# Performance work log

Measured on AMD Instinct MI355X. Metric: run time of the kernel, lower is better.

The kernel has to match this reference:

```python
import jax, jax.numpy as jnp
import numpy as np

N_NODES = 50000
N_EDGES = 800000
IN_CH = 128
HID = 64
OUT_CH = 2
NEG_SLOPE = 0.2


def gcn_conv(x, src, dst, deg_isqrt, W, b):
    # PyG GCNConv: x @ W, symmetric normalization with self-loops, scatter-add, + bias
    h = x @ W  # [N, HID]
    norm = deg_isqrt[src] * deg_isqrt[dst]  # [E+N]
    msg = h[src] * norm[:, None]  # gather + scale
    out = jax.ops.segment_sum(msg, dst, num_segments=x.shape[0])
    return out + b


def setup_inputs() -> dict:
    key = jax.random.key(0)
    ks = jax.random.split(key, 16)
    glorot = lambda k, i, o: jax.random.normal(k, (i, o), jnp.float32) * jnp.sqrt(2.0 / (i + o))
    inp = {
        "node_features": jax.random.normal(ks[0], (N_NODES, IN_CH), jnp.float32),
        "edge_index": jax.random.randint(ks[1], (2, N_EDGES), 0, N_NODES, jnp.int64 if jax.config.jax_enable_x64 else jnp.int32),
        "fc1_W": glorot(ks[2], IN_CH, 32), "fc1_b": jnp.zeros((32,), jnp.float32),
        "fc2_W": glorot(ks[3], 32, HID), "fc2_b": jnp.zeros((HID,), jnp.float32),
        "conv1_W": glorot(ks[4], HID, HID), "conv1_b": jnp.zeros((HID,), jnp.float32),
        "conv2_W": glorot(ks[5], HID, HID), "conv2_b": jnp.zeros((HID,), jnp.float32),
        "conv3_W": glorot(ks[6], HID, HID), "conv3_b": jnp.zeros((HID,), jnp.float32),
        "conv4_W": glorot(ks[7], HID, HID), "conv4_b": jnp.zeros((HID,), jnp.float32),
        "final_W": glorot(ks[8], HID, OUT_CH), "final_b": jnp.zeros((OUT_CH,), jnp.float32),
    }
    return inp


def reference(node_features, edge_index, fc1_W, fc1_b, fc2_W, fc2_b,
              conv1_W, conv1_b, conv2_W, conv2_b, conv3_W, conv3_b,
              conv4_W, conv4_b, final_W, final_b):
    N = node_features.shape[0]
    # add self-loops once (shared by all conv layers)
    loops = jnp.arange(N, dtype=edge_index.dtype)
    src = jnp.concatenate([edge_index[0], loops])
    dst = jnp.concatenate([edge_index[1], loops])
    deg = jax.ops.segment_sum(jnp.ones_like(dst, jnp.float32), dst, num_segments=N)
    deg_isqrt = jnp.where(deg > 0, jax.lax.rsqrt(jnp.maximum(deg, 1.0)), 0.0)

    lrelu = lambda x: jnp.where(x >= 0, x, NEG_SLOPE * x)

    x = jax.nn.relu(node_features @ fc1_W + fc1_b) @ fc2_W + fc2_b  # fc stack
    out1 = lrelu(gcn_conv(x, src, dst, deg_isqrt, conv1_W, conv1_b))
    out2 = lrelu(gcn_conv(out1, src, dst, deg_isqrt, conv2_W, conv2_b)) + out1
    out3 = lrelu(gcn_conv(out2, src, dst, deg_isqrt, conv3_W, conv3_b))
    out4 = gcn_conv(out3, src, dst, deg_isqrt, conv4_W, conv4_b) + out2
    return out4 @ final_W + final_b
```

## Files before the change

kernel.cpp:

```cpp
#include <hip/hip_runtime.h>

#define NN 50000
#define NE 800000
#define HIST_BLOCKS ((NE + 255) / 256)
#define FILL_BLOCKS HIST_BLOCKS
#define FC_BLOCKS 1024

typedef unsigned short u16;
typedef unsigned int u32;

__device__ inline float rlf(float v, int l) {
    return __int_as_float(__builtin_amdgcn_readlane(__float_as_int(v), l));
}
__device__ inline u16 f2bf(float f) {
    u32 u = __float_as_uint(f);
    u32 r = (u + 0x7FFFu + ((u >> 16) & 1u)) >> 16;
    return (u16)r;
}
__device__ inline float lo16(u32 q) { return __uint_as_float(q << 16); }
__device__ inline float hi16(u32 q) { return __uint_as_float(q & 0xffff0000u); }

__global__ __launch_bounds__(256) void k_hist_foldw(
    const int* __restrict__ dst, int* __restrict__ cnt,
    const float* __restrict__ fc2W, const float* __restrict__ b2,
    const float* __restrict__ c1W, float* __restrict__ W2c,
    float* __restrict__ b2c) {
    if (blockIdx.x < HIST_BLOCKS) {
        int e = blockIdx.x * 256 + threadIdx.x;
        if (e < NE) atomicAdd(&cnt[dst[e]], 1);
    } else {
        int j = (blockIdx.x - HIST_BLOCKS) * 4 + (threadIdx.x >> 6);
        int c = threadIdx.x & 63;
        if (j < 32) {
            float s = 0.f;
            for (int k = 0; k < 64; ++k) s = fmaf(fc2W[j * 64 + k], c1W[k * 64 + c], s);
            W2c[j * 64 + c] = s;
        } else if (j == 32) {
            float s = 0.f;
            for (int k = 0; k < 64; ++k) s = fmaf(b2[k], c1W[k * 64 + c], s);
            b2c[c] = s;
        }
    }
}

__global__ __launch_bounds__(1024) void k_scan(int* __restrict__ cnt,
                                               int* __restrict__ rowptr,
                                               float* __restrict__ disq) {
    __shared__ int wsum[16];
    __shared__ int carry;
    int t = threadIdx.x, wave = t >> 6, lane = t & 63;
    if (t == 0) { carry = 0; rowptr[0] = 0; }
    __syncthreads();
    for (int base = 0; base < NN; base += 1024) {
        int i = base + t;
        int x = (i < NN) ? cnt[i] : 0;
        if (i < NN) {
            cnt[i] = 0;
            disq[i] = rsqrtf((float)x + 1.0f);
        }
        for (int off = 1; off < 64; off <<= 1) {
            int y = __shfl_up(x, off, 64);
            if (lane >= off) x += y;
        }
        if (lane == 63) wsum[wave] = x;
        __syncthreads();
        if (wave == 0 && lane < 16) {
            int w = wsum[lane];
            for (int off = 1; off < 16; off <<= 1) {
                int y = __shfl_up(w, off, 16);
                if (lane >= off) w += y;
            }
            wsum[lane] = w;
        }
        __syncthreads();
        int incl = carry + ((wave > 0) ? wsum[wave - 1] : 0) + x;
        if (i < NN) rowptr[i + 1] = incl;
        __syncthreads();
        if (t == 1023) carry = incl;
        __syncthreads();
    }
}

__global__ __launch_bounds__(256) void k_fill_fc(
    const int* __restrict__ src, const int* __restrict__ dst,
    const int* __restrict__ rowptr, int* __restrict__ cur,
    u16* __restrict__ esrc,
    const float* __restrict__ nf,
    const float* __restrict__ W1, const float* __restrict__ b1,
    const float* __restrict__ W2c, const float* __restrict__ b2c,
    const float* __restrict__ disq, u16* __restrict__ Hb) {
    if (blockIdx.x < FILL_BLOCKS) {
        int e = blockIdx.x * 256 + threadIdx.x;
        if (e < NE) {
            int d = dst[e];
            int pos = rowptr[d] + atomicAdd(&cur[d], 1);
            esrc[pos] = (u16)src[e];
        }
        return;
    }
    int lane = threadIdx.x & 63;
    int c = lane & 31, h = lane >> 5;
    int wid = ((blockIdx.x - FILL_BLOCKS) * 256 + threadIdx.x) >> 6;
    int nwaves = (FC_BLOCKS * 256) >> 6;
    float w1[64], w2[32];
    #pragma unroll
    for (int j = 0; j < 64; ++j) w1[j] = W1[(h * 64 + j) * 32 + c];
    #pragma unroll
    for (int j = 0; j < 32; ++j) w2[j] = W2c[j * 64 + lane];
    float b1c = b1[c], b2l = b2c[lane];
    for (int n = wid; n < NN; n += nwaves) {
        float x0 = nf[(size_t)n * 128 + lane];
        float x1 = nf[(size_t)n * 128 + 64 + lane];
        float s = 0.f;
        #pragma unroll
        for (int j = 0; j < 64; ++j) {
            float xa = rlf(x0, j), xb = rlf(x1, j);
            s = fmaf(h ? xb : xa, w1[j], s);
        }
        s += __shfl_xor(s, 32, 64);
        float hv = fmaxf(s + b1c, 0.f);
        float o = b2l;
        #pragma unroll
        for (int j = 0; j < 32; ++j) o = fmaf(rlf(hv, j), w2[j], o);
        Hb[(size_t)n * 64 + lane] = f2bf(disq[n] * o);
    }
}

__global__ __launch_bounds__(256) void k_gemm64(
    const float* __restrict__ X, const float* __restrict__ W,
    const float* __restrict__ disq, u16* __restrict__ Hb) {
    int lane = threadIdx.x & 63;
    int wid = (blockIdx.x * 256 + threadIdx.x) >> 6;
    int nwaves = (gridDim.x * 256) >> 6;
    float wcol[64];
    #pragma unroll
    for (int k = 0; k < 64; ++k) wcol[k] = W[k * 64 + lane];
    for (int n = wid; n < NN; n += nwaves) {
        float xv = X[(size_t)n * 64 + lane];
        float acc = 0.f;
        #pragma unroll
        for (int k = 0; k < 64; ++k) acc = fmaf(rlf(xv, k), wcol[k], acc);
        Hb[(size_t)n * 64 + lane] = f2bf(disq[n] * acc);
    }
}

__global__ __launch_bounds__(256) void k_csr_conv(
    const u16* __restrict__ Hb, const int* __restrict__ rowptr,
    const u16* __restrict__ esrc, const float* __restrict__ disq,
    const float* __restrict__ b, const float* __restrict__ res,
    float* __restrict__ out, int do_lrelu) {
    int lane = threadIdx.x & 63;
    int half = lane >> 5;
    int cl = (lane & 31) * 2;
    int n = (blockIdx.x * 256 + threadIdx.x) >> 6;
    if (n >= NN) return;
    int beg = rowptr[n], end = rowptr[n + 1];
    float a0 = 0.f, a1 = 0.f;
    for (int base = beg; base < end; base += 64) {
        int cnt = min(64, end - base);
        int idx = (lane < cnt) ? (int)esrc[base + lane] : 0;
        int j = 0;
        for (; j + 8 <= cnt; j += 8) {
            int p0 = __builtin_amdgcn_readlane(idx, j + 0);
            int p1 = __builtin_amdgcn_readlane(idx, j + 1);
            int p2 = __builtin_amdgcn_readlane(idx, j + 2);
            int p3 = __builtin_amdgcn_readlane(idx, j + 3);
            int p4 = __builtin_amdgcn_readlane(idx, j + 4);
            int p5 = __builtin_amdgcn_readlane(idx, j + 5);
            int p6 = __builtin_amdgcn_readlane(idx, j + 6);
            int p7 = __builtin_amdgcn_readlane(idx, j + 7);
            int sA = half ? p1 : p0;
            int sB = half ? p3 : p2;
            int sC = half ? p5 : p4;
            int sD = half ? p7 : p6;
            u32 qA = *(const u32*)(Hb + ((size_t)sA * 64 + cl));
            u32 qB = *(const u32*)(Hb + ((size_t)sB * 64 + cl));
            u32 qC = *(const u32*)(Hb + ((size_t)sC * 64 + cl));
            u32 qD = *(const u32*)(Hb + ((size_t)sD * 64 + cl));
            a0 += (lo16(qA) + lo16(qB)) + (lo16(qC) + lo16(qD));
            a1 += (hi16(qA) + hi16(qB)) + (hi16(qC) + hi16(qD));
        }
        for (; j + 2 <= cnt; j += 2) {
            int p0 = __builtin_amdgcn_readlane(idx, j);
            int p1 = __builtin_amdgcn_readlane(idx, j + 1);
            int s = half ? p1 : p0;
            u32 q = *(const u32*)(Hb + ((size_t)s * 64 + cl));
            a0 += lo16(q);
            a1 += hi16(q);
        }
        if (j < cnt) {
            int s = __builtin_amdgcn_readlane(idx, j);
            if (!half) {
                u32 q = *(const u32*)(Hb + ((size_t)s * 64 + cl));
                a0 += lo16(q);
                a1 += hi16(q);
            }
        }
    }
    a0 += __shfl_xor(a0, 32, 64);
    a1 += __shfl_xor(a1, 32, 64);
    u32 qs = *(const u32*)(Hb + ((size_t)n * 64 + cl));
    a0 += lo16(qs);
    a1 += hi16(qs);
    float dn = disq[n];
    float v0 = dn * a0 + b[cl];
    float v1 = dn * a1 + b[cl + 1];
    if (do_lrelu) {
        v0 = (v0 >= 0.f) ? v0 : 0.2f * v0;
        v1 = (v1 >= 0.f) ? v1 : 0.2f * v1;
    }
    if (res) {
        float2 r = *(const float2*)(res + ((size_t)n * 64 + cl));
        v0 += r.x;
        v1 += r.y;
    }
    if (!half) {
        float2 o;
        o.x = v0;
        o.y = v1;
        *(float2*)(out + ((size_t)n * 64 + cl)) = o;
    }
}

__global__ __launch_bounds__(256) void k_csr_conv_final(
    const u16* __restrict__ Hb, const int* __restrict__ rowptr,
    const u16* __restrict__ esrc, const float* __restrict__ disq,
    const float* __restrict__ b, const float* __restrict__ res,
    const float* __restrict__ FW, const float* __restrict__ fb,
    float* __restrict__ out) {
    int lane = threadIdx.x & 63;
    int half = lane >> 5;
    int cl = (lane & 31) * 2;
    int n = (blockIdx.x * 256 + threadIdx.x) >> 6;
    if (n >= NN) return;
    int beg = rowptr[n], end = rowptr[n + 1];
    float a0 = 0.f, a1 = 0.f;
    for (int base = beg; base < end; base += 64) {
        int cnt = min(64, end - base);
        int idx = (lane < cnt) ? (int)esrc[base + lane] : 0;
        int j = 0;
        for (; j + 8 <= cnt; j += 8) {
            int p0 = __builtin_amdgcn_readlane(idx, j + 0);
            int p1 = __builtin_amdgcn_readlane(idx, j + 1);
            int p2 = __builtin_amdgcn_readlane(idx, j + 2);
            int p3 = __builtin_amdgcn_readlane(idx, j + 3);
            int p4 = __builtin_amdgcn_readlane(idx, j + 4);
            int p5 = __builtin_amdgcn_readlane(idx, j + 5);
            int p6 = __builtin_amdgcn_readlane(idx, j + 6);
            int p7 = __builtin_amdgcn_readlane(idx, j + 7);
            int sA = half ? p1 : p0;
            int sB = half ? p3 : p2;
            int sC = half ? p5 : p4;
            int sD = half ? p7 : p6;
            u32 qA = *(const u32*)(Hb + ((size_t)sA * 64 + cl));
            u32 qB = *(const u32*)(Hb + ((size_t)sB * 64 + cl));
            u32 qC = *(const u32*)(Hb + ((size_t)sC * 64 + cl));
            u32 qD = *(const u32*)(Hb + ((size_t)sD * 64 + cl));
            a0 += (lo16(qA) + lo16(qB)) + (lo16(qC) + lo16(qD));
            a1 += (hi16(qA) + hi16(qB)) + (hi16(qC) + hi16(qD));
        }
        for (; j + 2 <= cnt; j += 2) {
            int p0 = __builtin_amdgcn_readlane(idx, j);
            int p1 = __builtin_amdgcn_readlane(idx, j + 1);
            int s = half ? p1 : p0;
            u32 q = *(const u32*)(Hb + ((size_t)s * 64 + cl));
            a0 += lo16(q);
            a1 += hi16(q);
        }
        if (j < cnt) {
            int s = __builtin_amdgcn_readlane(idx, j);
            if (!half) {
                u32 q = *(const u32*)(Hb + ((size_t)s * 64 + cl));
                a0 += lo16(q);
                a1 += hi16(q);
            }
        }
    }
    a0 += __shfl_xor(a0, 32, 64);
    a1 += __shfl_xor(a1, 32, 64);
    u32 qs = *(const u32*)(Hb + ((size_t)n * 64 + cl));
    a0 += lo16(qs);
    a1 += hi16(qs);
    float dn = disq[n];
    float2 r = *(const float2*)(res + ((size_t)n * 64 + cl));
    float v0 = dn * a0 + b[cl] + r.x;
    float v1 = dn * a1 + b[cl + 1] + r.y;
    float p0 = v0 * FW[cl * 2 + 0] + v1 * FW[(cl + 1) * 2 + 0];
    float p1 = v0 * FW[cl * 2 + 1] + v1 * FW[(cl + 1) * 2 + 1];
    for (int off = 16; off; off >>= 1) {
        p0 += __shfl_xor(p0, off, 64);
        p1 += __shfl_xor(p1, off, 64);
    }
    if (lane == 0) {
        out[n * 2 + 0] = p0 + fb[0];
        out[n * 2 + 1] = p1 + fb[1];
    }
}

extern "C" void kernel_launch(void* const* d_in, const int* in_sizes, int n_in,
                              void* d_out, int out_size, void* d_ws, size_t ws_size,
                              hipStream_t stream) {
    const float* nf   = (const float*)d_in[0];
    const int*   ei   = (const int*)d_in[1];
    const float* fc1W = (const float*)d_in[2];
    const float* fc1b = (const float*)d_in[3];
    const float* fc2W = (const float*)d_in[4];
    const float* fc2b = (const float*)d_in[5];
    const float* cW[4] = {(const float*)d_in[6], (const float*)d_in[8],
                          (const float*)d_in[10], (const float*)d_in[12]};
    const float* cb[4] = {(const float*)d_in[7], (const float*)d_in[9],
                          (const float*)d_in[11], (const float*)d_in[13]};
    const float* fW = (const float*)d_in[14];
    const float* fb = (const float*)d_in[15];
    const int* src = ei;
    const int* dst = ei + NE;

    float* ws     = (float*)d_ws;
    float* disq   = ws;
    int*   cnt    = (int*)(ws + 50048);
    int*   rowptr = cnt + 50048;
    u16*   esrc   = (u16*)(rowptr + 50056);
    float* W2c    = (float*)(esrc + 800000);
    float* b2c    = W2c + 2048;
    float* B0     = b2c + 64;
    float* B1     = B0 + (size_t)NN * 64;
    u16*   Hb     = (u16*)(B1 + (size_t)NN * 64);

    hipMemsetAsync(cnt, 0, 50048 * sizeof(int), stream);
    k_hist_foldw<<<HIST_BLOCKS + 9, 256, 0, stream>>>(dst, cnt, fc2W, fc2b, cW[0],
                                                      W2c, b2c);
    k_scan<<<1, 1024, 0, stream>>>(cnt, rowptr, disq);
    k_fill_fc<<<FILL_BLOCKS + FC_BLOCKS, 256, 0, stream>>>(
        src, dst, rowptr, cnt, esrc, nf, fc1W, fc1b, W2c, b2c, disq, Hb);

    const int cgrid = (NN * 64 + 255) / 256;

    k_csr_conv<<<cgrid, 256, 0, stream>>>(Hb, rowptr, esrc, disq, cb[0], nullptr, B1, 1);
    k_gemm64<<<512, 256, 0, stream>>>(B1, cW[1], disq, Hb);
    k_csr_conv<<<cgrid, 256, 0, stream>>>(Hb, rowptr, esrc, disq, cb[1], B1, B0, 1);
    k_gemm64<<<512, 256, 0, stream>>>(B0, cW[2], disq, Hb);
    k_csr_conv<<<cgrid, 256, 0, stream>>>(Hb, rowptr, esrc, disq, cb[2], nullptr, B1, 1);
    k_gemm64<<<512, 256, 0, stream>>>(B1, cW[3], disq, Hb);
    k_csr_conv_final<<<cgrid, 256, 0, stream>>>(Hb, rowptr, esrc, disq, cb[3], B0,
                                                fW, fb, (float*)d_out);
}
```

Measured before the change: 353.4 us.

## Gather 4 edges per wave step with 8-byte loads and zero padding row

The CSR aggregation kernels now split each wave into four 16-lane quarters. Each quarter gathers a different neighbour row with an 8-byte load of 4 bf16 channels, instead of two halves each doing 4-byte loads. Out-of-range edge slots point at a zeroed padding row at index NN, which removes the tail branches, and the cross-quarter reduction uses two shuffles. The fill/fc kernel also interleaves its FC blocks among the fill blocks so the two kinds of work run together. This adds extra shuffles and padding-row loads on partial groups, and relies on the workspace having room for the extra Hb row.

After: 428.7 us. 1.21x slower.

```diff
diff --git a/kernel.cpp b/kernel.cpp
--- a/kernel.cpp
+++ b/kernel.cpp
@@ -45,11 +45,13 @@
 
 __global__ __launch_bounds__(1024) void k_scan(int* __restrict__ cnt,
                                                int* __restrict__ rowptr,
-                                               float* __restrict__ disq) {
+                                               float* __restrict__ disq,
+                                               u16* __restrict__ Hb) {
     __shared__ int wsum[16];
     __shared__ int carry;
     int t = threadIdx.x, wave = t >> 6, lane = t & 63;
     if (t == 0) { carry = 0; rowptr[0] = 0; }
+    if (t < 64) Hb[(size_t)NN * 64 + t] = 0;
     __syncthreads();
     for (int base = 0; base < NN; base += 1024) {
         int i = base + t;
@@ -89,8 +91,11 @@
     const float* __restrict__ W1, const float* __restrict__ b1,
     const float* __restrict__ W2c, const float* __restrict__ b2c,
     const float* __restrict__ disq, u16* __restrict__ Hb) {
-    if (blockIdx.x < FILL_BLOCKS) {
-        int e = blockIdx.x * 256 + threadIdx.x;
+    int b = blockIdx.x;
+    bool is_fc = ((b & 3) == 3) && ((b >> 2) < FC_BLOCKS);
+    if (!is_fc) {
+        int fillIdx = b - min(b >> 2, FC_BLOCKS);
+        int e = fillIdx * 256 + threadIdx.x;
         if (e < NE) {
             int d = dst[e];
             int pos = rowptr[d] + atomicAdd(&cur[d], 1);
@@ -100,7 +105,7 @@
     }
     int lane = threadIdx.x & 63;
     int c = lane & 31, h = lane >> 5;
-    int wid = ((blockIdx.x - FILL_BLOCKS) * 256 + threadIdx.x) >> 6;
+    int wid = ((b >> 2) * 256 + threadIdx.x) >> 6;
     int nwaves = (FC_BLOCKS * 256) >> 6;
     float w1[64], w2[32];
     #pragma unroll
@@ -144,81 +149,65 @@
     }
 }
 
+#define GRP(J)                                                              \
+    {                                                                       \
+        int p0 = __builtin_amdgcn_readlane(idx, (J) + 0);                   \
+        int p1 = __builtin_amdgcn_readlane(idx, (J) + 1);                   \
+        int p2 = __builtin_amdgcn_readlane(idx, (J) + 2);                   \
+        int p3 = __builtin_amdgcn_readlane(idx, (J) + 3);                   \
+        int s = (q == 0) ? p0 : ((q == 1) ? p1 : ((q == 2) ? p2 : p3));     \
+        uint2 v = *(const uint2*)(Hb + (((size_t)s) << 6) + c4);            \
+        a0 += lo16(v.x);                                                    \
+        a1 += hi16(v.x);                                                    \
+        a2 += lo16(v.y);                                                    \
+        a3 += hi16(v.y);                                                    \
+    }
+
 __global__ __launch_bounds__(256) void k_csr_conv(
     const u16* __restrict__ Hb, const int* __restrict__ rowptr,
     const u16* __restrict__ esrc, const float* __restrict__ disq,
     const float* __restrict__ b, const float* __restrict__ res,
     float* __restrict__ out, int do_lrelu) {
     int lane = threadIdx.x & 63;
-    int half = lane >> 5;
-    int cl = (lane & 31) * 2;
+    int q = lane >> 4;
+    int c4 = (lane & 15) * 4;
     int n = (blockIdx.x * 256 + threadIdx.x) >> 6;
     if (n >= NN) return;
     int beg = rowptr[n], end = rowptr[n + 1];
-    float a0 = 0.f, a1 = 0.f;
+    float a0 = 0.f, a1 = 0.f, a2 = 0.f, a3 = 0.f;
     for (int base = beg; base < end; base += 64) {
-        int cnt = min(64, end - base);
-        int idx = (lane < cnt) ? (int)esrc[base + lane] : 0;
+        int cnt64 = min(64, end - base);
+        int idx = (lane < cnt64) ? (int)esrc[base + lane] : NN;
         int j = 0;
-        for (; j + 8 <= cnt; j += 8) {
-            int p0 = __builtin_amdgcn_readlane(idx, j + 0);
-            int p1 = __builtin_amdgcn_readlane(idx, j + 1);
-            int p2 = __builtin_amdgcn_readlane(idx, j + 2);
-            int p3 = __builtin_amdgcn_readlane(idx, j + 3);
-            int p4 = __builtin_amdgcn_readlane(idx, j + 4);
-            int p5 = __builtin_amdgcn_readlane(idx, j + 5);
-            int p6 = __builtin_amdgcn_readlane(idx, j + 6);
-            int p7 = __builtin_amdgcn_readlane(idx, j + 7);
-            int sA = half ? p1 : p0;
-            int sB = half ? p3 : p2;
-            int sC = half ? p5 : p4;
-            int sD = half ? p7 : p6;
-            u32 qA = *(const u32*)(Hb + ((size_t)sA * 64 + cl));
-            u32 qB = *(const u32*)(Hb + ((size_t)sB * 64 + cl));
-            u32 qC = *(const u32*)(Hb + ((size_t)sC * 64 + cl));
-            u32 qD = *(const u32*)(Hb + ((size_t)sD * 64 + cl));
-            a0 += (lo16(qA) + lo16(qB)) + (lo16(qC) + lo16(qD));
-            a1 += (hi16(qA) + hi16(qB)) + (hi16(qC) + hi16(qD));
-        }
-        for (; j + 2 <= cnt; j += 2) {
-            int p0 = __builtin_amdgcn_readlane(idx, j);
-            int p1 = __builtin_amdgcn_readlane(idx, j + 1);
-            int s = half ? p1 : p0;
-            u32 q = *(const u32*)(Hb + ((size_t)s * 64 + cl));
-            a0 += lo16(q);
-            a1 += hi16(q);
-        }
-        if (j < cnt) {
-            int s = __builtin_amdgcn_readlane(idx, j);
-            if (!half) {
-                u32 q = *(const u32*)(Hb + ((size_t)s * 64 + cl));
-                a0 += lo16(q);
-                a1 += hi16(q);
-            }
-        }
-    }
-    a0 += __shfl_xor(a0, 32, 64);
-    a1 += __shfl_xor(a1, 32, 64);
-    u32 qs = *(const u32*)(Hb + ((size_t)n * 64 + cl));
-    a0 += lo16(qs);
-    a1 += hi16(qs);
-    float dn = disq[n];
-    float v0 = dn * a0 + b[cl];
-    float v1 = dn * a1 + b[cl + 1];
-    if (do_lrelu) {
-        v0 = (v0 >= 0.f) ? v0 : 0.2f * v0;
-        v1 = (v1 >= 0.f) ? v1 : 0.2f * v1;
-    }
-    if (res) {
-        float2 r = *(const float2*)(res + ((size_t)n * 64 + cl));
-        v0 += r.x;
-        v1 += r.y;
-    }
-    if (!half) {
-        float2 o;
-        o.x = v0;
-        o.y = v1;
-        *(float2*)(out + ((size_t)n * 64 + cl)) = o;
+        for (; j + 16 <= cnt64; j += 16) { GRP(j) GRP(j + 4) GRP(j + 8) GRP(j + 12) }
+        for (; j < cnt64; j += 4) { GRP(j) }
+    }
+    a0 += __shfl_xor(a0, 16, 64); a0 += __shfl_xor(a0, 32, 64);
+    a1 += __shfl_xor(a1, 16, 64); a1 += __shfl_xor(a1, 32, 64);
+    a2 += __shfl_xor(a2, 16, 64); a2 += __shfl_xor(a2, 32, 64);
+    a3 += __shfl_xor(a3, 16, 64); a3 += __shfl_xor(a3, 32, 64);
+    if (q == 0) {
+        uint2 sv = *(const uint2*)(Hb + (((size_t)n) << 6) + c4);
+        a0 += lo16(sv.x); a1 += hi16(sv.x); a2 += lo16(sv.y); a3 += hi16(sv.y);
+        float dn = disq[n];
+        float4 bv = *(const float4*)(b + c4);
+        float v0 = dn * a0 + bv.x;
+        float v1 = dn * a1 + bv.y;
+        float v2 = dn * a2 + bv.z;
+        float v3 = dn * a3 + bv.w;
+        if (do_lrelu) {
+            v0 = (v0 >= 0.f) ? v0 : 0.2f * v0;
+            v1 = (v1 >= 0.f) ? v1 : 0.2f * v1;
+            v2 = (v2 >= 0.f) ? v2 : 0.2f * v2;
+            v3 = (v3 >= 0.f) ? v3 : 0.2f * v3;
+        }
+        if (res) {
+            float4 r = *(const float4*)(res + (((size_t)n) << 6) + c4);
+            v0 += r.x; v1 += r.y; v2 += r.z; v3 += r.w;
+        }
+        float4 o;
+        o.x = v0; o.y = v1; o.z = v2; o.w = v3;
+        *(float4*)(out + (((size_t)n) << 6) + c4) = o;
     }
 }
 
@@ -229,65 +218,37 @@
     const float* __restrict__ FW, const float* __restrict__ fb,
     float* __restrict__ out) {
     int lane = threadIdx.x & 63;
-    int half = lane >> 5;
-    int cl = (lane & 31) * 2;
+    int q = lane >> 4;
+    int c4 = (lane & 15) * 4;
     int n = (blockIdx.x * 256 + threadIdx.x) >> 6;
     if (n >= NN) return;
     int beg = rowptr[n], end = rowptr[n + 1];
-    float a0 = 0.f, a1 = 0.f;
+    float a0 = 0.f, a1 = 0.f, a2 = 0.f, a3 = 0.f;
     for (int base = beg; base < end; base += 64) {
-        int cnt = min(64, end - base);
-        int idx = (lane < cnt) ? (int)esrc[base + lane] : 0;
+        int cnt64 = min(64, end - base);
+        int idx = (lane < cnt64) ? (int)esrc[base + lane] : NN;
         int j = 0;
-        for (; j + 8 <= cnt; j += 8) {
-            int p0 = __builtin_amdgcn_readlane(idx, j + 0);
-            int p1 = __builtin_amdgcn_readlane(idx, j + 1);
-            int p2 = __builtin_amdgcn_readlane(idx, j + 2);
-            int p3 = __builtin_amdgcn_readlane(idx, j + 3);
-            int p4 = __builtin_amdgcn_readlane(idx, j + 4);
-            int p5 = __builtin_amdgcn_readlane(idx, j + 5);
-            int p6 = __builtin_amdgcn_readlane(idx, j + 6);
-            int p7 = __builtin_amdgcn_readlane(idx, j + 7);
-            int sA = half ? p1 : p0;
-            int sB = half ? p3 : p2;
-            int sC = half ? p5 : p4;
-            int sD = half ? p7 : p6;
-            u32 qA = *(const u32*)(Hb + ((size_t)sA * 64 + cl));
-            u32 qB = *(const u32*)(Hb + ((size_t)sB * 64 + cl));
-            u32 qC = *(const u32*)(Hb + ((size_t)sC * 64 + cl));
-            u32 qD = *(const u32*)(Hb + ((size_t)sD * 64 + cl));
-            a0 += (lo16(qA) + lo16(qB)) + (lo16(qC) + lo16(qD));
-            a1 += (hi16(qA) + hi16(qB)) + (hi16(qC) + hi16(qD));
-        }
-        for (; j + 2 <= cnt; j += 2) {
-            int p0 = __builtin_amdgcn_readlane(idx, j);
-            int p1 = __builtin_amdgcn_readlane(idx, j + 1);
-            int s = half ? p1 : p0;
-            u32 q = *(const u32*)(Hb + ((size_t)s * 64 + cl));
-            a0 += lo16(q);
-            a1 += hi16(q);
-        }
-        if (j < cnt) {
-            int s = __builtin_amdgcn_readlane(idx, j);
-            if (!half) {
-                u32 q = *(const u32*)(Hb + ((size_t)s * 64 + cl));
-                a0 += lo16(q);
-                a1 += hi16(q);
-            }
-        }
-    }
-    a0 += __shfl_xor(a0, 32, 64);
-    a1 += __shfl_xor(a1, 32, 64);
-    u32 qs = *(const u32*)(Hb + ((size_t)n * 64 + cl));
-    a0 += lo16(qs);
-    a1 += hi16(qs);
+        for (; j + 16 <= cnt64; j += 16) { GRP(j) GRP(j + 4) GRP(j + 8) GRP(j + 12) }
+        for (; j < cnt64; j += 4) { GRP(j) }
+    }
+    a0 += __shfl_xor(a0, 16, 64); a0 += __shfl_xor(a0, 32, 64);
+    a1 += __shfl_xor(a1, 16, 64); a1 += __shfl_xor(a1, 32, 64);
+    a2 += __shfl_xor(a2, 16, 64); a2 += __shfl_xor(a2, 32, 64);
+    a3 += __shfl_xor(a3, 16, 64); a3 += __shfl_xor(a3, 32, 64);
+    uint2 sv = *(const uint2*)(Hb + (((size_t)n) << 6) + c4);
+    a0 += lo16(sv.x); a1 += hi16(sv.x); a2 += lo16(sv.y); a3 += hi16(sv.y);
     float dn = disq[n];
-    float2 r = *(const float2*)(res + ((size_t)n * 64 + cl));
-    float v0 = dn * a0 + b[cl] + r.x;
-    float v1 = dn * a1 + b[cl + 1] + r.y;
-    float p0 = v0 * FW[cl * 2 + 0] + v1 * FW[(cl + 1) * 2 + 0];
-    float p1 = v0 * FW[cl * 2 + 1] + v1 * FW[(cl + 1) * 2 + 1];
-    for (int off = 16; off; off >>= 1) {
+    float4 bv = *(const float4*)(b + c4);
+    float4 r = *(const float4*)(res + (((size_t)n) << 6) + c4);
+    float v0 = dn * a0 + bv.x + r.x;
+    float v1 = dn * a1 + bv.y + r.y;
+    float v2 = dn * a2 + bv.z + r.z;
+    float v3 = dn * a3 + bv.w + r.w;
+    float4 f01 = *(const float4*)(FW + c4 * 2);
+    float4 f23 = *(const float4*)(FW + c4 * 2 + 4);
+    float p0 = v0 * f01.x + v1 * f01.z + v2 * f23.x + v3 * f23.z;
+    float p1 = v0 * f01.y + v1 * f01.w + v2 * f23.y + v3 * f23.w;
+    for (int off = 1; off < 16; off <<= 1) {
         p0 += __shfl_xor(p0, off, 64);
         p1 += __shfl_xor(p1, off, 64);
     }
@@ -329,7 +290,7 @@
     hipMemsetAsync(cnt, 0, 50048 * sizeof(int), stream);
     k_hist_foldw<<<HIST_BLOCKS + 9, 256, 0, stream>>>(dst, cnt, fc2W, fc2b, cW[0],
                                                       W2c, b2c);
-    k_scan<<<1, 1024, 0, stream>>>(cnt, rowptr, disq);
+    k_scan<<<1, 1024, 0, stream>>>(cnt, rowptr, disq, Hb);
     k_fill_fc<<<FILL_BLOCKS + FC_BLOCKS, 256, 0, stream>>>(
         src, dst, rowptr, cnt, esrc, nf, fc1W, fc1b, W2c, b2c, disq, Hb);
 
```
